# Kernel tuning notes

Hardware: AMD Instinct MI355X
Metric: run time of the kernel (lower is better)

## Reference

```python
import jax, jax.numpy as jnp
import numpy as np

DEG_CLAMP = 1e6  # matches .clamp(max=1000000.0) on deg^-0.5


def setup_inputs() -> dict:
    key = jax.random.key(0)
    k1, k2, k3 = jax.random.split(key, 3)
    N, E, D_IN, D_OUT = 100000, 1600000, 128, 128
    x = jax.random.normal(k1, (N, D_IN), dtype=jnp.float32)
    edge_index = jax.random.randint(k2, (2, E), 0, N, dtype=jnp.int64)
    # Linear params (xavier_uniform on weight, zero-ish bias)
    limit = float(np.sqrt(6.0 / (D_IN + D_OUT)))
    W = jax.random.uniform(k3, (D_OUT, D_IN), dtype=jnp.float32, minval=-limit, maxval=limit)
    b = jnp.zeros((D_OUT,), dtype=jnp.float32)
    return {"x": x, "edge_index": edge_index, "W": W, "b": b}


def reference(x, edge_index, W, b):
    N = x.shape[0]
    # append self-loops: ei = cat([edge_index, [arange(N); arange(N)]], dim=1)
    self_idx = jnp.arange(N, dtype=edge_index.dtype)
    src = jnp.concatenate([edge_index[0], self_idx])  # [E+N]
    dst = jnp.concatenate([edge_index[1], self_idx])  # [E+N]
    # degree of destination nodes (with self-loops)
    deg = jax.ops.segment_sum(jnp.ones_like(dst, dtype=x.dtype), dst, num_segments=N)
    deg_inv_sqrt = jnp.minimum(deg ** -0.5, DEG_CLAMP)
    # linear transform (dropout is identity in eval)
    h = x @ W.T + b  # [N, D_OUT]
    # symmetric normalization, gather, scale, scatter-add
    norm = deg_inv_sqrt[src] * deg_inv_sqrt[dst]  # [E+N]
    msgs = h[src] * norm[:, None]                  # [E+N, D_OUT]
    out = jax.ops.segment_sum(msgs, dst, num_segments=N)  # [N, D_OUT]
    return out
```

## Files before the change

### kernel.cpp

```cpp
#include <hip/hip_runtime.h>
#include <hip/hip_bf16.h>
#include <cstddef>

#define D 128
#define SHIFT 9
#define RN (1 << SHIFT)
#define CAPLOG 14
#define CAP (1 << CAPLOG)

typedef __attribute__((ext_vector_type(8))) short bf16x8;
typedef __attribute__((ext_vector_type(16))) float f32x16;
typedef __attribute__((ext_vector_type(4))) float f32x4;

static __device__ __forceinline__ unsigned short f2bf(float f) {
  return __builtin_bit_cast(unsigned short, __float2bfloat16(f));
}
static __device__ __forceinline__ float bflo(unsigned u) {
  return __uint_as_float(u << 16);
}
static __device__ __forceinline__ float bfhi(unsigned u) {
  return __uint_as_float(u & 0xffff0000u);
}

__global__ void k_init(int* __restrict__ gcursor, int nc, unsigned* __restrict__ gz) {
  const int t = threadIdx.x;
  if (t < nc) gcursor[t] = t << CAPLOG;
  if (t < 64) gz[t] = 0;
}

__global__ __launch_bounds__(256) void k_psort(
    const int* __restrict__ src, const int* __restrict__ dst,
    int* __restrict__ gcursor, unsigned* __restrict__ pairs, int e, int nc) {
  __shared__ int hist4[4][256];
  const int tid = threadIdx.x;
  const int w = tid >> 6;
  const int base = blockIdx.x * 4096;
  const int m = min(4096, e - base);
#pragma unroll
  for (int u = 0; u < 4; ++u) ((int*)hist4)[tid + 256 * u] = 0;
  __syncthreads();
  int myd[16], mys[16];
#pragma unroll
  for (int j = 0; j < 16; ++j) {
    const int i = tid + j * 256;
    if (i < m) {
      myd[j] = dst[base + i];
      mys[j] = src[base + i];
      atomicAdd(&hist4[w][myd[j] >> SHIFT], 1);
    }
  }
  __syncthreads();
  if (tid < nc) {
    const int t0 = hist4[0][tid], t1 = hist4[1][tid];
    const int t2 = hist4[2][tid], t3 = hist4[3][tid];
    const int tot = t0 + t1 + t2 + t3;
    int b = (tot > 0) ? atomicAdd(&gcursor[tid], tot) : 0;
    hist4[0][tid] = b;
    hist4[1][tid] = b + t0;
    hist4[2][tid] = b + t0 + t1;
    hist4[3][tid] = b + t0 + t1 + t2;
  }
  __syncthreads();
#pragma unroll
  for (int j = 0; j < 16; ++j) {
    const int i = tid + j * 256;
    if (i < m) {
      const int c = myd[j] >> SHIFT;
      const int pos = atomicAdd(&hist4[w][c], 1);
      const unsigned pk = (unsigned)mys[j] | ((unsigned)(myd[j] & (RN - 1)) << 22);
      __builtin_nontemporal_store(pk, &pairs[pos]);
    }
  }
}

__global__ __launch_bounds__(512) void k_fine(
    const unsigned* __restrict__ pairs, const int* __restrict__ gcursor,
    int* __restrict__ rowptr, int* __restrict__ cnt, float* __restrict__ dinv,
    int* __restrict__ srcs, int n) {
  __shared__ int hist[RN];
  __shared__ int rowL[RN];
  __shared__ int sdata[RN];
  const int c = blockIdx.x;
  const int tid = threadIdx.x;
  const int node0 = c << SHIFT;
  const int nodes = min(RN, n - node0);
  hist[tid] = 0;
  __syncthreads();
  const int beg = c << CAPLOG;
  const int end = gcursor[c];
  for (int i = beg + tid; i < end; i += RN)
    atomicAdd(&hist[pairs[i] >> 22], 1);
  __syncthreads();
  const int deg = hist[tid];
  const int p = (deg + 7) & ~7;
  sdata[tid] = p;
  __syncthreads();
  for (int off = 1; off < RN; off <<= 1) {
    int t = (tid >= off) ? sdata[tid - off] : 0;
    __syncthreads();
    sdata[tid] += t;
    __syncthreads();
  }
  const int rbase = beg + sdata[tid] - p;
  rowL[tid] = rbase;
  hist[tid] = rbase;
  if (tid < nodes) {
    rowptr[node0 + tid] = rbase;
    cnt[node0 + tid] = p;
    dinv[node0 + tid] = fminf(rsqrtf((float)(deg + 1)), 1.0e6f);
  }
  __syncthreads();
  for (int i = beg + tid; i < end; i += RN) {
    const unsigned pr = pairs[i];
    const int pos = atomicAdd(&hist[pr >> 22], 1);
    srcs[pos] = (int)(pr & 0x3FFFFFu);
  }
  __syncthreads();
  const int fend = rowL[tid] + p;
  for (int i = hist[tid]; i < fend; ++i) srcs[i] = n;
}

__global__ __launch_bounds__(256) void k_gemm(
    const float* __restrict__ x, const float* __restrict__ W,
    const float* __restrict__ bias, const float* __restrict__ dinv,
    __hip_bfloat16* __restrict__ g, int n) {
  __shared__ unsigned short xs[128 * 128];
  __shared__ unsigned short Ws[128 * 128];
  const int tid = threadIdx.x;
  const int row0 = blockIdx.x * 128;

#pragma unroll
  for (int u = 0; u < 8; ++u) {
    const int f = tid + 256 * u;
    const int row = f >> 4;
    const int c = f & 15;
    const int ch = (c ^ (row & 7)) << 3;
    {
      const float4* p = reinterpret_cast<const float4*>(&W[(size_t)row * D + c * 8]);
      const float4 v0 = p[0], v1 = p[1];
      uint4 pk;
      pk.x = f2bf(v0.x) | ((unsigned)f2bf(v0.y) << 16);
      pk.y = f2bf(v0.z) | ((unsigned)f2bf(v0.w) << 16);
      pk.z = f2bf(v1.x) | ((unsigned)f2bf(v1.y) << 16);
      pk.w = f2bf(v1.z) | ((unsigned)f2bf(v1.w) << 16);
      *reinterpret_cast<uint4*>(&Ws[row * 128 + ch]) = pk;
    }
    {
      float4 v0 = make_float4(0.f, 0.f, 0.f, 0.f), v1 = v0;
      if (row0 + row < n) {
        const float4* p =
            reinterpret_cast<const float4*>(&x[(size_t)(row0 + row) * D + c * 8]);
        v0 = p[0]; v1 = p[1];
      }
      uint4 pk;
      pk.x = f2bf(v0.x) | ((unsigned)f2bf(v0.y) << 16);
      pk.y = f2bf(v0.z) | ((unsigned)f2bf(v0.w) << 16);
      pk.z = f2bf(v1.x) | ((unsigned)f2bf(v1.y) << 16);
      pk.w = f2bf(v1.z) | ((unsigned)f2bf(v1.w) << 16);
      *reinterpret_cast<uint4*>(&xs[row * 128 + ch]) = pk;
    }
  }
  __syncthreads();

  const int lane = tid & 63;
  const int wv = tid >> 6;
  const int wr = (wv >> 1) * 64;
  const int wc = (wv & 1) * 64;
  const int lr = lane & 31;
  const int lk = lane >> 5;

  f32x16 acc[2][2];
#pragma unroll
  for (int m = 0; m < 2; ++m)
#pragma unroll
    for (int j = 0; j < 2; ++j)
#pragma unroll
      for (int q = 0; q < 16; ++q) acc[m][j][q] = 0.f;

#pragma unroll
  for (int ks = 0; ks < 8; ++ks) {
    bf16x8 a[2], b[2];
#pragma unroll
    for (int m = 0; m < 2; ++m) {
      const int r = wr + m * 32 + lr;
      const int ch = ((ks * 2 + lk) ^ (r & 7)) << 3;
      a[m] = *reinterpret_cast<const bf16x8*>(&xs[r * 128 + ch]);
    }
#pragma unroll
    for (int j = 0; j < 2; ++j) {
      const int r = wc + j * 32 + lr;
      const int ch = ((ks * 2 + lk) ^ (r & 7)) << 3;
      b[j] = *reinterpret_cast<const bf16x8*>(&Ws[r * 128 + ch]);
    }
#pragma unroll
    for (int m = 0; m < 2; ++m)
#pragma unroll
      for (int j = 0; j < 2; ++j)
        acc[m][j] = __builtin_amdgcn_mfma_f32_32x32x16_bf16(a[m], b[j], acc[m][j], 0, 0, 0);
  }

#pragma unroll
  for (int m = 0; m < 2; ++m) {
#pragma unroll
    for (int reg = 0; reg < 16; ++reg) {
      const int rloc = (reg & 3) + 8 * (reg >> 2) + 4 * lk;
      const int r = row0 + wr + m * 32 + rloc;
      if (r < n) {
        const float dv = dinv[r];
#pragma unroll
        for (int j = 0; j < 2; ++j) {
          const int col = wc + j * 32 + lr;
          g[(size_t)r * D + col] = __float2bfloat16((acc[m][j][reg] + bias[col]) * dv);
        }
      }
    }
  }
}

__global__ __launch_bounds__(256) void k_accum(
    const int* __restrict__ rowptr, const int* __restrict__ cnt,
    const int* __restrict__ srcs, const uint2* __restrict__ gq,
    const float* __restrict__ dinv, float* __restrict__ out, int n) {
  const int w = (int)(((size_t)blockIdx.x * 256 + threadIdx.x) >> 6);
  const int lane = threadIdx.x & 63;
  if (w >= n) return;
  const int li = lane & 31;
  const int half = lane >> 5;
  const int beg = rowptr[w];
  const int num = cnt[w];

  const uint2 sv = gq[(size_t)(half ? n : w) * 32 + li];
  float a0 = bflo(sv.x), a1 = bfhi(sv.x), a2 = bflo(sv.y), a3 = bfhi(sv.y);

  if (num > 0) {
    const int2* s2 = (const int2*)(srcs + beg);
    int2 sp0 = s2[0], sp1 = s2[1], sp2 = s2[2], sp3 = s2[3];
    for (int k = 0; k < num; k += 8) {
      const int nxt = (k + 8 < num) ? (beg + k + 8) : beg;
      const int2* s2n = (const int2*)(srcs + nxt);
      const int2 np0 = s2n[0], np1 = s2n[1], np2 = s2n[2], np3 = s2n[3];
      const int e0 = half ? sp0.y : sp0.x;
      const int e1 = half ? sp1.y : sp1.x;
      const int e2 = half ? sp2.y : sp2.x;
      const int e3 = half ? sp3.y : sp3.x;
      const uint2 t0 = gq[(size_t)e0 * 32 + li];
      const uint2 t1 = gq[(size_t)e1 * 32 + li];
      const uint2 t2 = gq[(size_t)e2 * 32 + li];
      const uint2 t3 = gq[(size_t)e3 * 32 + li];
      a0 += bflo(t0.x) + bflo(t1.x) + bflo(t2.x) + bflo(t3.x);
      a1 += bfhi(t0.x) + bfhi(t1.x) + bfhi(t2.x) + bfhi(t3.x);
      a2 += bflo(t0.y) + bflo(t1.y) + bflo(t2.y) + bflo(t3.y);
      a3 += bfhi(t0.y) + bfhi(t1.y) + bfhi(t2.y) + bfhi(t3.y);
      sp0 = np0; sp1 = np1; sp2 = np2; sp3 = np3;
    }
  }

  a0 += __shfl_xor(a0, 32);
  a1 += __shfl_xor(a1, 32);
  a2 += __shfl_xor(a2, 32);
  a3 += __shfl_xor(a3, 32);

  if (!half) {
    const float dv = dinv[w];
    f32x4 res;
    res[0] = a0 * dv; res[1] = a1 * dv; res[2] = a2 * dv; res[3] = a3 * dv;
    f32x4* dst = (f32x4*)(out + (size_t)w * D) + li;
    __builtin_nontemporal_store(res, dst);
  }
}

extern "C" void kernel_launch(void* const* d_in, const int* in_sizes, int n_in,
                              void* d_out, int out_size, void* d_ws, size_t ws_size,
                              hipStream_t stream) {
  const float* x = (const float*)d_in[0];
  const int* ei = (const int*)d_in[1];
  const float* W = (const float*)d_in[2];
  const float* b = (const float*)d_in[3];
  float* out = (float*)d_out;
  const int n = in_sizes[0] / D;
  const int e = in_sizes[1] / 2;
  const int* src = ei;
  const int* dst = ei + e;
  const int nc = (n + RN - 1) >> SHIFT;

  char* ws = (char*)d_ws;
  const size_t nbb = ((size_t)n * 4 + 255) / 256 * 256;
  const size_t pb = (((size_t)nc << CAPLOG) * 4 + 255) / 256 * 256;
  float* dinv = (float*)ws;
  int* rowptr = (int*)(ws + nbb);
  int* cnt = (int*)(ws + 2 * nbb);
  int* gcursor = (int*)(ws + 3 * nbb);
  int* srcs = (int*)(ws + 3 * nbb + 1024);
  char* pr_base = ws + 3 * nbb + 1024 + pb;
  unsigned* pairs = (unsigned*)pr_base;
  __hip_bfloat16* g = (__hip_bfloat16*)pr_base;

  k_init<<<1, 256, 0, stream>>>(gcursor, nc, (unsigned*)(g + (size_t)n * D));
  k_psort<<<(e + 4095) / 4096, 256, 0, stream>>>(src, dst, gcursor, pairs, e, nc);
  k_fine<<<nc, RN, 0, stream>>>(pairs, gcursor, rowptr, cnt, dinv, srcs, n);
  k_gemm<<<(n + 127) / 128, 256, 0, stream>>>(x, W, b, dinv, g, n);
  k_accum<<<(n + 3) / 4, 256, 0, stream>>>(rowptr, cnt, srcs, (const uint2*)g,
                                           dinv, out, n);
}
```

Measured before the change: 179.5 us.

## Pre-convert W to bf16, vectorize GEMM output stores, widen gather unroll to 8

W is converted to bf16 once in the init kernel, so each GEMM block copies bf16 W instead of re-converting fp32. The GEMM operands are swapped (W as A, x as B) so each lane holds four consecutive output columns and can store packed 8-byte bf16 chunks instead of scattered 2-byte stores. The accumulate loop now reads int4 index chunks and issues 8 gathers per half-wave per iteration, with rows padded to multiples of 16. The extra padding increases dummy-row gathers for low-degree nodes.

```diff
diff --git a/kernel.cpp b/kernel.cpp
--- a/kernel.cpp
+++ b/kernel.cpp
@@ -22,10 +22,12 @@
   return __uint_as_float(u & 0xffff0000u);
 }
 
-__global__ void k_init(int* __restrict__ gcursor, int nc, unsigned* __restrict__ gz) {
-  const int t = threadIdx.x;
+__global__ void k_init(int* __restrict__ gcursor, int nc, unsigned* __restrict__ gz,
+                       const float* __restrict__ W, unsigned short* __restrict__ Wbf) {
+  const int t = blockIdx.x * 256 + threadIdx.x;
   if (t < nc) gcursor[t] = t << CAPLOG;
   if (t < 64) gz[t] = 0;
+  if (t < 128 * 128) Wbf[t] = f2bf(W[t]);
 }
 
 __global__ __launch_bounds__(256) void k_psort(
@@ -92,7 +94,7 @@
     atomicAdd(&hist[pairs[i] >> 22], 1);
   __syncthreads();
   const int deg = hist[tid];
-  const int p = (deg + 7) & ~7;
+  const int p = (deg + 15) & ~15;
   sdata[tid] = p;
   __syncthreads();
   for (int off = 1; off < RN; off <<= 1) {
@@ -121,7 +123,7 @@
 }
 
 __global__ __launch_bounds__(256) void k_gemm(
-    const float* __restrict__ x, const float* __restrict__ W,
+    const float* __restrict__ x, const unsigned short* __restrict__ Wbf,
     const float* __restrict__ bias, const float* __restrict__ dinv,
     __hip_bfloat16* __restrict__ g, int n) {
   __shared__ unsigned short xs[128 * 128];
@@ -135,82 +137,78 @@
     const int row = f >> 4;
     const int c = f & 15;
     const int ch = (c ^ (row & 7)) << 3;
-    {
-      const float4* p = reinterpret_cast<const float4*>(&W[(size_t)row * D + c * 8]);
-      const float4 v0 = p[0], v1 = p[1];
-      uint4 pk;
-      pk.x = f2bf(v0.x) | ((unsigned)f2bf(v0.y) << 16);
-      pk.y = f2bf(v0.z) | ((unsigned)f2bf(v0.w) << 16);
-      pk.z = f2bf(v1.x) | ((unsigned)f2bf(v1.y) << 16);
-      pk.w = f2bf(v1.z) | ((unsigned)f2bf(v1.w) << 16);
-      *reinterpret_cast<uint4*>(&Ws[row * 128 + ch]) = pk;
-    }
-    {
-      float4 v0 = make_float4(0.f, 0.f, 0.f, 0.f), v1 = v0;
-      if (row0 + row < n) {
-        const float4* p =
-            reinterpret_cast<const float4*>(&x[(size_t)(row0 + row) * D + c * 8]);
-        v0 = p[0]; v1 = p[1];
-      }
-      uint4 pk;
-      pk.x = f2bf(v0.x) | ((unsigned)f2bf(v0.y) << 16);
-      pk.y = f2bf(v0.z) | ((unsigned)f2bf(v0.w) << 16);
-      pk.z = f2bf(v1.x) | ((unsigned)f2bf(v1.y) << 16);
-      pk.w = f2bf(v1.z) | ((unsigned)f2bf(v1.w) << 16);
-      *reinterpret_cast<uint4*>(&xs[row * 128 + ch]) = pk;
-    }
+    *reinterpret_cast<uint4*>(&Ws[row * 128 + ch]) =
+        *reinterpret_cast<const uint4*>(&Wbf[row * 128 + c * 8]);
+    float4 v0 = make_float4(0.f, 0.f, 0.f, 0.f), v1 = v0;
+    if (row0 + row < n) {
+      const float4* p =
+          reinterpret_cast<const float4*>(&x[(size_t)(row0 + row) * D + c * 8]);
+      v0 = p[0]; v1 = p[1];
+    }
+    uint4 pk;
+    pk.x = f2bf(v0.x) | ((unsigned)f2bf(v0.y) << 16);
+    pk.y = f2bf(v0.z) | ((unsigned)f2bf(v0.w) << 16);
+    pk.z = f2bf(v1.x) | ((unsigned)f2bf(v1.y) << 16);
+    pk.w = f2bf(v1.z) | ((unsigned)f2bf(v1.w) << 16);
+    *reinterpret_cast<uint4*>(&xs[row * 128 + ch]) = pk;
   }
   __syncthreads();
 
   const int lane = tid & 63;
   const int wv = tid >> 6;
-  const int wr = (wv >> 1) * 64;
-  const int wc = (wv & 1) * 64;
+  const int xr0 = (wv >> 1) * 64;
+  const int cc0 = (wv & 1) * 64;
   const int lr = lane & 31;
   const int lk = lane >> 5;
 
   f32x16 acc[2][2];
 #pragma unroll
-  for (int m = 0; m < 2; ++m)
-#pragma unroll
-    for (int j = 0; j < 2; ++j)
-#pragma unroll
-      for (int q = 0; q < 16; ++q) acc[m][j][q] = 0.f;
+  for (int p = 0; p < 2; ++p)
+#pragma unroll
+    for (int q = 0; q < 2; ++q)
+#pragma unroll
+      for (int t = 0; t < 16; ++t) acc[p][q][t] = 0.f;
 
 #pragma unroll
   for (int ks = 0; ks < 8; ++ks) {
     bf16x8 a[2], b[2];
 #pragma unroll
-    for (int m = 0; m < 2; ++m) {
-      const int r = wr + m * 32 + lr;
+    for (int p = 0; p < 2; ++p) {
+      const int r = cc0 + p * 32 + lr;
       const int ch = ((ks * 2 + lk) ^ (r & 7)) << 3;
-      a[m] = *reinterpret_cast<const bf16x8*>(&xs[r * 128 + ch]);
-    }
-#pragma unroll
-    for (int j = 0; j < 2; ++j) {
-      const int r = wc + j * 32 + lr;
+      a[p] = *reinterpret_cast<const bf16x8*>(&Ws[r * 128 + ch]);
+    }
+#pragma unroll
+    for (int q = 0; q < 2; ++q) {
+      const int r = xr0 + q * 32 + lr;
       const int ch = ((ks * 2 + lk) ^ (r & 7)) << 3;
-      b[j] = *reinterpret_cast<const bf16x8*>(&Ws[r * 128 + ch]);
-    }
-#pragma unroll
-    for (int m = 0; m < 2; ++m)
-#pragma unroll
-      for (int j = 0; j < 2; ++j)
-        acc[m][j] = __builtin_amdgcn_mfma_f32_32x32x16_bf16(a[m], b[j], acc[m][j], 0, 0, 0);
-  }
-
-#pragma unroll
-  for (int m = 0; m < 2; ++m) {
-#pragma unroll
-    for (int reg = 0; reg < 16; ++reg) {
-      const int rloc = (reg & 3) + 8 * (reg >> 2) + 4 * lk;
-      const int r = row0 + wr + m * 32 + rloc;
-      if (r < n) {
-        const float dv = dinv[r];
-#pragma unroll
-        for (int j = 0; j < 2; ++j) {
-          const int col = wc + j * 32 + lr;
-          g[(size_t)r * D + col] = __float2bfloat16((acc[m][j][reg] + bias[col]) * dv);
+      b[q] = *reinterpret_cast<const bf16x8*>(&xs[r * 128 + ch]);
+    }
+#pragma unroll
+    for (int p = 0; p < 2; ++p)
+#pragma unroll
+      for (int q = 0; q < 2; ++q)
+        acc[p][q] = __builtin_amdgcn_mfma_f32_32x32x16_bf16(a[p], b[q], acc[p][q], 0, 0, 0);
+  }
+
+#pragma unroll
+  for (int q = 0; q < 2; ++q) {
+    const int r = row0 + xr0 + q * 32 + lr;
+    if (r < n) {
+      const float dv = dinv[r];
+#pragma unroll
+      for (int p = 0; p < 2; ++p) {
+#pragma unroll
+        for (int rg = 0; rg < 4; ++rg) {
+          const int cb = cc0 + p * 32 + 8 * rg + 4 * lk;
+          const float v0 = (acc[p][q][rg * 4 + 0] + bias[cb + 0]) * dv;
+          const float v1 = (acc[p][q][rg * 4 + 1] + bias[cb + 1]) * dv;
+          const float v2 = (acc[p][q][rg * 4 + 2] + bias[cb + 2]) * dv;
+          const float v3 = (acc[p][q][rg * 4 + 3] + bias[cb + 3]) * dv;
+          uint2 pk;
+          pk.x = f2bf(v0) | ((unsigned)f2bf(v1) << 16);
+          pk.y = f2bf(v2) | ((unsigned)f2bf(v3) << 16);
+          *reinterpret_cast<uint2*>(&g[(size_t)r * D + cb]) = pk;
         }
       }
     }
@@ -233,25 +231,32 @@
   float a0 = bflo(sv.x), a1 = bfhi(sv.x), a2 = bflo(sv.y), a3 = bfhi(sv.y);
 
   if (num > 0) {
-    const int2* s2 = (const int2*)(srcs + beg);
-    int2 sp0 = s2[0], sp1 = s2[1], sp2 = s2[2], sp3 = s2[3];
-    for (int k = 0; k < num; k += 8) {
-      const int nxt = (k + 8 < num) ? (beg + k + 8) : beg;
-      const int2* s2n = (const int2*)(srcs + nxt);
-      const int2 np0 = s2n[0], np1 = s2n[1], np2 = s2n[2], np3 = s2n[3];
-      const int e0 = half ? sp0.y : sp0.x;
-      const int e1 = half ? sp1.y : sp1.x;
-      const int e2 = half ? sp2.y : sp2.x;
-      const int e3 = half ? sp3.y : sp3.x;
+    const int4* s4 = (const int4*)(srcs + beg);
+    int4 q0 = s4[0], q1 = s4[1], q2 = s4[2], q3 = s4[3];
+    for (int k = 0; k < num; k += 16) {
+      const int nx = (k + 16 < num) ? ((k + 16) >> 2) : 0;
+      const int4 n0 = s4[nx], n1 = s4[nx + 1], n2 = s4[nx + 2], n3 = s4[nx + 3];
+      const int e0 = half ? q0.y : q0.x, e1 = half ? q0.w : q0.z;
+      const int e2 = half ? q1.y : q1.x, e3 = half ? q1.w : q1.z;
+      const int e4 = half ? q2.y : q2.x, e5 = half ? q2.w : q2.z;
+      const int e6 = half ? q3.y : q3.x, e7 = half ? q3.w : q3.z;
       const uint2 t0 = gq[(size_t)e0 * 32 + li];
       const uint2 t1 = gq[(size_t)e1 * 32 + li];
       const uint2 t2 = gq[(size_t)e2 * 32 + li];
       const uint2 t3 = gq[(size_t)e3 * 32 + li];
-      a0 += bflo(t0.x) + bflo(t1.x) + bflo(t2.x) + bflo(t3.x);
-      a1 += bfhi(t0.x) + bfhi(t1.x) + bfhi(t2.x) + bfhi(t3.x);
-      a2 += bflo(t0.y) + bflo(t1.y) + bflo(t2.y) + bflo(t3.y);
-      a3 += bfhi(t0.y) + bfhi(t1.y) + bfhi(t2.y) + bfhi(t3.y);
-      sp0 = np0; sp1 = np1; sp2 = np2; sp3 = np3;
+      const uint2 t4 = gq[(size_t)e4 * 32 + li];
+      const uint2 t5 = gq[(size_t)e5 * 32 + li];
+      const uint2 t6 = gq[(size_t)e6 * 32 + li];
+      const uint2 t7 = gq[(size_t)e7 * 32 + li];
+      a0 += bflo(t0.x) + bflo(t1.x) + bflo(t2.x) + bflo(t3.x) +
+            bflo(t4.x) + bflo(t5.x) + bflo(t6.x) + bflo(t7.x);
+      a1 += bfhi(t0.x) + bfhi(t1.x) + bfhi(t2.x) + bfhi(t3.x) +
+            bfhi(t4.x) + bfhi(t5.x) + bfhi(t6.x) + bfhi(t7.x);
+      a2 += bflo(t0.y) + bflo(t1.y) + bflo(t2.y) + bflo(t3.y) +
+            bflo(t4.y) + bflo(t5.y) + bflo(t6.y) + bflo(t7.y);
+      a3 += bfhi(t0.y) + bfhi(t1.y) + bfhi(t2.y) + bfhi(t3.y) +
+            bfhi(t4.y) + bfhi(t5.y) + bfhi(t6.y) + bfhi(t7.y);
+      q0 = n0; q1 = n1; q2 = n2; q3 = n3;
     }
   }
 
@@ -290,15 +295,16 @@
   int* rowptr = (int*)(ws + nbb);
   int* cnt = (int*)(ws + 2 * nbb);
   int* gcursor = (int*)(ws + 3 * nbb);
-  int* srcs = (int*)(ws + 3 * nbb + 1024);
-  char* pr_base = ws + 3 * nbb + 1024 + pb;
+  unsigned short* Wbf = (unsigned short*)(ws + 3 * nbb + 1024);
+  int* srcs = (int*)(ws + 3 * nbb + 1024 + 32768);
+  char* pr_base = ws + 3 * nbb + 1024 + 32768 + pb;
   unsigned* pairs = (unsigned*)pr_base;
   __hip_bfloat16* g = (__hip_bfloat16*)pr_base;
 
-  k_init<<<1, 256, 0, stream>>>(gcursor, nc, (unsigned*)(g + (size_t)n * D));
+  k_init<<<64, 256, 0, stream>>>(gcursor, nc, (unsigned*)(g + (size_t)n * D), W, Wbf);
   k_psort<<<(e + 4095) / 4096, 256, 0, stream>>>(src, dst, gcursor, pairs, e, nc);
   k_fine<<<nc, RN, 0, stream>>>(pairs, gcursor, rowptr, cnt, dinv, srcs, n);
-  k_gemm<<<(n + 127) / 128, 256, 0, stream>>>(x, W, b, dinv, g, n);
+  k_gemm<<<(n + 127) / 128, 256, 0, stream>>>(x, Wbf, b, dinv, g, n);
   k_accum<<<(n + 3) / 4, 256, 0, stream>>>(rowptr, cnt, srcs, (const uint2*)g,
                                            dinv, out, n);
 }
```

Result: no change. 176.1 us, median of 2 (-1.9%).
